# Kernel tuning notes

Measured on AMD Instinct MI355X. Metric: run time of the kernel, lower is better.

The kernel has to match this reference:

```python
import jax, jax.numpy as jnp
import numpy as np

N_NODES = 50000
N_EDGES = 800000
D_IN = 128
D_OUT = 128


def setup_inputs() -> dict:
    key = jax.random.key(0)
    ks = jax.random.split(key, 10)
    x = jax.random.normal(ks[0], (N_NODES, D_IN), dtype=jnp.float32)
    lp_rows = jax.random.randint(ks[1], (N_EDGES,), 0, N_NODES, dtype=jnp.int32)
    lp_cols = jax.random.randint(ks[2], (N_EDGES,), 0, N_NODES, dtype=jnp.int32)
    # low-pass operator: positive normalized-adjacency-like weights
    lp_vals = jax.random.uniform(ks[3], (N_EDGES,), dtype=jnp.float32) / 16.0
    hp_rows = jax.random.randint(ks[4], (N_EDGES,), 0, N_NODES, dtype=jnp.int32)
    hp_cols = jax.random.randint(ks[5], (N_EDGES,), 0, N_NODES, dtype=jnp.int32)
    # high-pass operator: signed (Laplacian-like) weights
    hp_vals = jax.random.normal(ks[6], (N_EDGES,), dtype=jnp.float32) / 16.0
    alpha_w = jax.random.normal(ks[7], (1, D_IN), dtype=jnp.float32) * 0.05
    alpha_b = jnp.zeros((1,), dtype=jnp.float32)
    W = jax.random.normal(ks[8], (D_OUT, D_IN), dtype=jnp.float32) * (1.0 / np.sqrt(D_IN))
    b = jnp.zeros((D_OUT,), dtype=jnp.float32)
    return {"x": x, "lp_rows": lp_rows, "lp_cols": lp_cols, "lp_vals": lp_vals,
            "hp_rows": hp_rows, "hp_cols": hp_cols, "hp_vals": hp_vals,
            "alpha_w": alpha_w, "alpha_b": alpha_b, "W": W, "b": b}


def _spmm(rows, cols, vals, x, n):
    # COO sparse-dense matmul: out[r] += vals[e] * x[cols[e]]
    return jax.ops.segment_sum(vals[:, None] * x[cols], rows, num_segments=n)


def reference(x, lp_rows, lp_cols, lp_vals, hp_rows, hp_cols, hp_vals,
              alpha_w, alpha_b, W, b):
    n = x.shape[0]
    # per-node mixing gate: alpha_i = sigmoid(x_i . theta + b)  -> [N, 1]
    alpha = jax.nn.sigmoid(x @ alpha_w.T + alpha_b)
    z_lp = _spmm(lp_rows, lp_cols, lp_vals, x, n)   # [N, D_IN]
    z_hp = _spmm(hp_rows, hp_cols, hp_vals, x, n)   # [N, D_IN]
    z_mix = alpha * z_lp + (1.0 - alpha) * z_hp
    out = jax.nn.relu(z_mix @ W.T + b)              # use_activation=True
    return out, alpha
```

## Files before the change

kernel.cpp:

```cpp
#include <hip/hip_runtime.h>

#define N_NODES_C 50000
#define N_EDGES_C 800000
#define N_EDGES2_C (2 * N_EDGES_C)
#define D 128
#define NSHARD 8
#define OFCAP 4096

#define BROWS 4
#define NBKT (N_NODES_C / BROWS)
#define NSB (NSHARD * NBKT)
#define BCAP 32

#define GNODES 64
#define LDP 132
#define GGRID ((N_NODES_C + GNODES - 1) / GNODES)
#define FGRID 2048
#define FEPB ((N_EDGES2_C + FGRID - 1) / FGRID)
#define TOTG (GGRID + FGRID)

static __device__ __forceinline__ unsigned short f2bf(float f) {
  unsigned u = __float_as_uint(f);
  u += 0x7fff + ((u >> 16) & 1);
  return (unsigned short)(u >> 16);
}
static __device__ __forceinline__ float bf_lo(unsigned u) {
  return __uint_as_float(u << 16);
}
static __device__ __forceinline__ float bf_hi(unsigned u) {
  return __uint_as_float(u & 0xffff0000u);
}

static __device__ __forceinline__ int xcd_id() {
  int v;
  asm volatile("s_getreg_b32 %0, hwreg(HW_REG_XCC_ID, 0, 4)" : "=s"(v));
  return v & (NSHARD - 1);
}

__global__ __launch_bounds__(256) void alpha_zero_kernel(
    const float* __restrict__ x,
    const float* __restrict__ aw,
    const float* __restrict__ ab,
    float* __restrict__ alpha_out,
    float* __restrict__ alpha_ws,
    int* __restrict__ bcursor,
    int n) {
  int gtid = blockIdx.x * blockDim.x + threadIdx.x;
  if (gtid < NSB + 64) bcursor[gtid] = 0;

  int wave = gtid >> 6;
  int lane = threadIdx.x & 63;
  if (wave >= n) return;
  const float* xr = x + (size_t)wave * D;
  float s = xr[lane] * aw[lane] + xr[lane + 64] * aw[lane + 64];
  #pragma unroll
  for (int off = 32; off > 0; off >>= 1)
    s += __shfl_down(s, off);
  if (lane == 0) {
    float a = 1.0f / (1.0f + __expf(-(s + ab[0])));
    alpha_out[wave] = a;
    alpha_ws[wave] = a;
  }
}

__global__ __launch_bounds__(256) void gemm_fill_kernel(
    const float* __restrict__ x,
    const float* __restrict__ W,
    unsigned* __restrict__ y,
    const int* __restrict__ lp_rows, const int* __restrict__ lp_cols,
    const float* __restrict__ lp_vals,
    const int* __restrict__ hp_rows, const int* __restrict__ hp_cols,
    const float* __restrict__ hp_vals,
    const float* __restrict__ alpha,
    int* __restrict__ bcursor,
    uint2* __restrict__ bins,
    int* __restrict__ ofcnt,
    uint2* __restrict__ ofl,
    int n) {
  __shared__ float zs[GNODES][LDP];
  __shared__ float wt[64][LDP];

  int t = threadIdx.x;
  int bid = blockIdx.x;
  int g = (bid * GGRID) / TOTG;
  int gn = ((bid + 1) * GGRID) / TOTG;

  if (gn > g) {
    int node0 = g * GNODES;
    int tn = t & 15;
    int tjg = t >> 4;
    int jb = tjg * 4;

    #pragma unroll
    for (int it = 0; it < 8; ++it) {
      int f = t + it * 256;
      int r = f >> 5;
      int c4 = f & 31;
      int node = node0 + r;
      float4 v = make_float4(0.f, 0.f, 0.f, 0.f);
      if (node < n) v = ((const float4*)(x + (size_t)node * D))[c4];
      *(float4*)&zs[r][c4 * 4] = v;
    }

    for (int jh = 0; jh < 2; ++jh) {
      if (jh) __syncthreads();
      #pragma unroll
      for (int it = 0; it < 8; ++it) {
        int f = t + it * 256;
        int j = f >> 5;
        int k4 = f & 31;
        *(float4*)&wt[j][k4 * 4] =
            ((const float4*)W)[(size_t)(jh * 64 + j) * 32 + k4];
      }
      __syncthreads();

      float acc[4][4] = {};
      #pragma unroll 2
      for (int k = 0; k < D; k += 4) {
        float4 w0 = *(const float4*)&wt[jb + 0][k];
        float4 w1 = *(const float4*)&wt[jb + 1][k];
        float4 w2 = *(const float4*)&wt[jb + 2][k];
        float4 w3 = *(const float4*)&wt[jb + 3][k];
        float4 z0 = *(const float4*)&zs[tn][k];
        float4 z1 = *(const float4*)&zs[tn + 16][k];
        float4 z2 = *(const float4*)&zs[tn + 32][k];
        float4 z3 = *(const float4*)&zs[tn + 48][k];
        acc[0][0] += z0.x*w0.x + z0.y*w0.y + z0.z*w0.z + z0.w*w0.w;
        acc[0][1] += z0.x*w1.x + z0.y*w1.y + z0.z*w1.z + z0.w*w1.w;
        acc[0][2] += z0.x*w2.x + z0.y*w2.y + z0.z*w2.z + z0.w*w2.w;
        acc[0][3] += z0.x*w3.x + z0.y*w3.y + z0.z*w3.z + z0.w*w3.w;
        acc[1][0] += z1.x*w0.x + z1.y*w0.y + z1.z*w0.z + z1.w*w0.w;
        acc[1][1] += z1.x*w1.x + z1.y*w1.y + z1.z*w1.z + z1.w*w1.w;
        acc[1][2] += z1.x*w2.x + z1.y*w2.y + z1.z*w2.z + z1.w*w2.w;
        acc[1][3] += z1.x*w3.x + z1.y*w3.y + z1.z*w3.z + z1.w*w3.w;
        acc[2][0] += z2.x*w0.x + z2.y*w0.y + z2.z*w0.z + z2.w*w0.w;
        acc[2][1] += z2.x*w1.x + z2.y*w1.y + z2.z*w1.z + z2.w*w1.w;
        acc[2][2] += z2.x*w2.x + z2.y*w2.y + z2.z*w2.z + z2.w*w2.w;
        acc[2][3] += z2.x*w3.x + z2.y*w3.y + z2.z*w3.z + z2.w*w3.w;
        acc[3][0] += z3.x*w0.x + z3.y*w0.y + z3.z*w0.z + z3.w*w0.w;
        acc[3][1] += z3.x*w1.x + z3.y*w1.y + z3.z*w1.z + z3.w*w1.w;
        acc[3][2] += z3.x*w2.x + z3.y*w2.y + z3.z*w2.z + z3.w*w2.w;
        acc[3][3] += z3.x*w3.x + z3.y*w3.y + z3.z*w3.z + z3.w*w3.w;
      }

      #pragma unroll
      for (int ii = 0; ii < 4; ++ii) {
        int node = node0 + ii * 16 + tn;
        if (node < n) {
          uint2 o;
          o.x = (unsigned)f2bf(acc[ii][0]) | ((unsigned)f2bf(acc[ii][1]) << 16);
          o.y = (unsigned)f2bf(acc[ii][2]) | ((unsigned)f2bf(acc[ii][3]) << 16);
          *(uint2*)&y[(size_t)node * 64 + jh * 32 + tjg * 2] = o;
        }
      }
    }
  } else {
    int fb = bid - g;
    int xcc = xcd_id();
    int e0 = fb * FEPB;
    int e1 = e0 + FEPB;
    if (e1 > N_EDGES2_C) e1 = N_EDGES2_C;
    for (int e = e0 + t; e < e1; e += 256) {
      int r, c;
      float v;
      if (e < N_EDGES_C) {
        r = __builtin_nontemporal_load(lp_rows + e);
        c = __builtin_nontemporal_load(lp_cols + e);
        v = __builtin_nontemporal_load(lp_vals + e) * alpha[r];
      } else {
        int i = e - N_EDGES_C;
        r = __builtin_nontemporal_load(hp_rows + i);
        c = __builtin_nontemporal_load(hp_cols + i);
        v = __builtin_nontemporal_load(hp_vals + i) * (1.0f - alpha[r]);
      }
      int sb = xcc * NBKT + (r >> 2);
      int p = atomicAdd(&bcursor[sb], 1);
      if (p < BCAP) {
        bins[(size_t)sb * BCAP + p] =
            make_uint2(((unsigned)r << 16) | (unsigned)c, __float_as_uint(v));
      } else {
        int q = atomicAdd(ofcnt, 1);
        if (q < OFCAP)
          ofl[q] = make_uint2(((unsigned)r << 16) | (unsigned)c,
                              (unsigned)__float_as_int(v));
      }
    }
  }
}

__global__ __launch_bounds__(256) void gather_kernel(
    const int* __restrict__ bcursor,
    const uint2* __restrict__ bins,
    const unsigned* __restrict__ y,
    const float* __restrict__ bias,
    const int* __restrict__ ofcnt,
    const uint2* __restrict__ ofl,
    float* __restrict__ out) {
  int t = threadIdx.x;
  int w = t >> 6;
  int lane = t & 63;
  int bkt = blockIdx.x * 4 + w;

  float a0L = 0.f, a0H = 0.f, a1L = 0.f, a1H = 0.f;
  float a2L = 0.f, a2H = 0.f, a3L = 0.f, a3H = 0.f;

  #define ACC(RR, VV, UU)                                        \
    do {                                                         \
      float uL_ = bf_lo(UU), uH_ = bf_hi(UU);                    \
      switch (RR) {                                              \
        case 0: a0L += (VV) * uL_; a0H += (VV) * uH_; break;     \
        case 1: a1L += (VV) * uL_; a1H += (VV) * uH_; break;     \
        case 2: a2L += (VV) * uL_; a2H += (VV) * uH_; break;     \
        default: a3L += (VV) * uL_; a3H += (VV) * uH_; break;    \
      }                                                          \
    } while (0)

  int cnts[8];
  uint2 wvs[8];
  #pragma unroll
  for (int s = 0; s < 8; ++s) {
    int c = bcursor[s * NBKT + bkt];
    cnts[s] = c > BCAP ? BCAP : c;
  }
  #pragma unroll
  for (int s = 0; s < 8; ++s) {
    wvs[s] = make_uint2(0u, 0u);
    if (lane < cnts[s])
      wvs[s] = bins[(size_t)(s * NBKT + bkt) * BCAP + lane];
  }

  #pragma unroll
  for (int s = 0; s < 8; ++s) {
    int cnt = cnts[s];
    uint2 wv = wvs[s];
    int i = 0;
    for (; i + 3 < cnt; i += 4) {
      unsigned x0 = (unsigned)__shfl((int)wv.x, i + 0);
      unsigned x1 = (unsigned)__shfl((int)wv.x, i + 1);
      unsigned x2 = (unsigned)__shfl((int)wv.x, i + 2);
      unsigned x3 = (unsigned)__shfl((int)wv.x, i + 3);
      float v0 = __uint_as_float((unsigned)__shfl((int)wv.y, i + 0));
      float v1 = __uint_as_float((unsigned)__shfl((int)wv.y, i + 1));
      float v2 = __uint_as_float((unsigned)__shfl((int)wv.y, i + 2));
      float v3 = __uint_as_float((unsigned)__shfl((int)wv.y, i + 3));
      unsigned u0 = y[(size_t)(x0 & 0xffffu) * 64 + lane];
      unsigned u1 = y[(size_t)(x1 & 0xffffu) * 64 + lane];
      unsigned u2 = y[(size_t)(x2 & 0xffffu) * 64 + lane];
      unsigned u3 = y[(size_t)(x3 & 0xffffu) * 64 + lane];
      int r0 = (int)__builtin_amdgcn_readfirstlane((x0 >> 16) & 3);
      int r1 = (int)__builtin_amdgcn_readfirstlane((x1 >> 16) & 3);
      int r2 = (int)__builtin_amdgcn_readfirstlane((x2 >> 16) & 3);
      int r3 = (int)__builtin_amdgcn_readfirstlane((x3 >> 16) & 3);
      ACC(r0, v0, u0);
      ACC(r1, v1, u1);
      ACC(r2, v2, u2);
      ACC(r3, v3, u3);
    }
    for (; i < cnt; ++i) {
      unsigned x0 = (unsigned)__shfl((int)wv.x, i);
      float v0 = __uint_as_float((unsigned)__shfl((int)wv.y, i));
      unsigned u0 = y[(size_t)(x0 & 0xffffu) * 64 + lane];
      int r0 = (int)__builtin_amdgcn_readfirstlane((x0 >> 16) & 3);
      ACC(r0, v0, u0);
    }
  }

  int nof = *ofcnt;
  if (nof > OFCAP) nof = OFCAP;
  for (int i = 0; i < nof; ++i) {
    uint2 o = ofl[i];
    unsigned r = o.x >> 16;
    if ((int)(r >> 2) == bkt) {
      unsigned u = y[(size_t)(o.x & 0xffffu) * 64 + lane];
      float v = __int_as_float((int)o.y);
      ACC((int)(r & 3), v, u);
    }
  }
  #undef ACC

  float2 bv = *(const float2*)&bias[lane * 2];
  size_t ro = (size_t)bkt * 4 * D + lane * 2;
  float2 o0, o1, o2, o3;
  o0.x = fmaxf(a0L + bv.x, 0.0f); o0.y = fmaxf(a0H + bv.y, 0.0f);
  o1.x = fmaxf(a1L + bv.x, 0.0f); o1.y = fmaxf(a1H + bv.y, 0.0f);
  o2.x = fmaxf(a2L + bv.x, 0.0f); o2.y = fmaxf(a2H + bv.y, 0.0f);
  o3.x = fmaxf(a3L + bv.x, 0.0f); o3.y = fmaxf(a3H + bv.y, 0.0f);
  *(float2*)&out[ro + 0 * D] = o0;
  *(float2*)&out[ro + 1 * D] = o1;
  *(float2*)&out[ro + 2 * D] = o2;
  *(float2*)&out[ro + 3 * D] = o3;
}

extern "C" void kernel_launch(void* const* d_in, const int* in_sizes, int n_in,
                              void* d_out, int out_size, void* d_ws, size_t ws_size,
                              hipStream_t stream) {
  const float* x = (const float*)d_in[0];
  const int* lp_rows = (const int*)d_in[1];
  const int* lp_cols = (const int*)d_in[2];
  const float* lp_vals = (const float*)d_in[3];
  const int* hp_rows = (const int*)d_in[4];
  const int* hp_cols = (const int*)d_in[5];
  const float* hp_vals = (const float*)d_in[6];
  const float* alpha_w = (const float*)d_in[7];
  const float* alpha_b = (const float*)d_in[8];
  const float* W = (const float*)d_in[9];
  const float* bias = (const float*)d_in[10];

  float* out = (float*)d_out;
  float* alpha_out = out + (size_t)N_NODES_C * D;

  char* ws = (char*)d_ws;
  unsigned* y = (unsigned*)ws;   ws += (size_t)N_NODES_C * 64 * 4;
  float* alpha_ws = (float*)ws;  ws += 200192;
  int* bcursor = (int*)ws;       ws += (size_t)NSB * 4;
  int* ofcnt = (int*)ws;         ws += 256;
  uint2* ofl = (uint2*)ws;       ws += (size_t)OFCAP * 8;
  uint2* bins = (uint2*)ws;
  ws += (size_t)NSB * BCAP * 8;

  alpha_zero_kernel<<<(N_NODES_C + 3) / 4, 256, 0, stream>>>(
      x, alpha_w, alpha_b, alpha_out, alpha_ws, bcursor, N_NODES_C);

  gemm_fill_kernel<<<TOTG, 256, 0, stream>>>(
      x, W, y,
      lp_rows, lp_cols, lp_vals, hp_rows, hp_cols, hp_vals,
      alpha_ws, bcursor, bins, ofcnt, ofl, N_NODES_C);

  gather_kernel<<<NBKT / 4, 256, 0, stream>>>(
      bcursor, bins, (const unsigned*)y, bias, ofcnt, ofl, out);
}
```

Baseline: 274.5 us.

## Fold alpha gate into GEMM blocks and apply alpha in gather via tag bit

Moves the per-node sigmoid gate computation out of the standalone first kernel and into the GEMM blocks of the fused gemm/fill kernel. The first kernel now only zeroes the bucket cursors with int4 stores. Edge values no longer carry alpha, which removes the random alpha[r] read during binning. Instead, the low bit of each stored value marks the edge as low-pass or high-pass, and the gather kernel multiplies by alpha or 1-alpha for the row it already owns. This lets the fill blocks run without waiting on the alpha computation, but it perturbs the value's lowest mantissa bit and adds a select and multiply per edge in the gather loop.

```diff
diff --git a/kernel.cpp b/kernel.cpp
--- a/kernel.cpp
+++ b/kernel.cpp
@@ -37,41 +37,23 @@
   return v & (NSHARD - 1);
 }
 
-__global__ __launch_bounds__(256) void alpha_zero_kernel(
+__global__ __launch_bounds__(256) void zero_kernel(int4* __restrict__ p) {
+  int g = blockIdx.x * 256 + threadIdx.x;
+  if (g < (NSB + 64) / 4) p[g] = make_int4(0, 0, 0, 0);
+}
+
+__global__ __launch_bounds__(256) void gemm_fill_kernel(
     const float* __restrict__ x,
+    const float* __restrict__ W,
     const float* __restrict__ aw,
     const float* __restrict__ ab,
     float* __restrict__ alpha_out,
     float* __restrict__ alpha_ws,
-    int* __restrict__ bcursor,
-    int n) {
-  int gtid = blockIdx.x * blockDim.x + threadIdx.x;
-  if (gtid < NSB + 64) bcursor[gtid] = 0;
-
-  int wave = gtid >> 6;
-  int lane = threadIdx.x & 63;
-  if (wave >= n) return;
-  const float* xr = x + (size_t)wave * D;
-  float s = xr[lane] * aw[lane] + xr[lane + 64] * aw[lane + 64];
-  #pragma unroll
-  for (int off = 32; off > 0; off >>= 1)
-    s += __shfl_down(s, off);
-  if (lane == 0) {
-    float a = 1.0f / (1.0f + __expf(-(s + ab[0])));
-    alpha_out[wave] = a;
-    alpha_ws[wave] = a;
-  }
-}
-
-__global__ __launch_bounds__(256) void gemm_fill_kernel(
-    const float* __restrict__ x,
-    const float* __restrict__ W,
     unsigned* __restrict__ y,
     const int* __restrict__ lp_rows, const int* __restrict__ lp_cols,
     const float* __restrict__ lp_vals,
     const int* __restrict__ hp_rows, const int* __restrict__ hp_cols,
     const float* __restrict__ hp_vals,
-    const float* __restrict__ alpha,
     int* __restrict__ bcursor,
     uint2* __restrict__ bins,
     int* __restrict__ ofcnt,
@@ -154,6 +136,25 @@
         }
       }
     }
+
+    int wv = t >> 6;
+    int ln = t & 63;
+    float bb = ab[0];
+    for (int ii = 0; ii < 16; ++ii) {
+      int node = node0 + wv * 16 + ii;
+      if (node < n) {
+        const float* xr = x + (size_t)node * D;
+        float s = xr[ln] * aw[ln] + xr[ln + 64] * aw[ln + 64];
+        #pragma unroll
+        for (int off = 32; off > 0; off >>= 1)
+          s += __shfl_down(s, off);
+        if (ln == 0) {
+          float a = 1.0f / (1.0f + __expf(-(s + bb)));
+          alpha_out[node] = a;
+          alpha_ws[node] = a;
+        }
+      }
+    }
   } else {
     int fb = bid - g;
     int xcc = xcd_id();
@@ -162,27 +163,26 @@
     if (e1 > N_EDGES2_C) e1 = N_EDGES2_C;
     for (int e = e0 + t; e < e1; e += 256) {
       int r, c;
-      float v;
+      unsigned vb;
       if (e < N_EDGES_C) {
         r = __builtin_nontemporal_load(lp_rows + e);
         c = __builtin_nontemporal_load(lp_cols + e);
-        v = __builtin_nontemporal_load(lp_vals + e) * alpha[r];
+        vb = (__float_as_uint(__builtin_nontemporal_load(lp_vals + e)) & ~1u) | 1u;
       } else {
         int i = e - N_EDGES_C;
         r = __builtin_nontemporal_load(hp_rows + i);
         c = __builtin_nontemporal_load(hp_cols + i);
-        v = __builtin_nontemporal_load(hp_vals + i) * (1.0f - alpha[r]);
+        vb = __float_as_uint(__builtin_nontemporal_load(hp_vals + i)) & ~1u;
       }
       int sb = xcc * NBKT + (r >> 2);
       int p = atomicAdd(&bcursor[sb], 1);
       if (p < BCAP) {
         bins[(size_t)sb * BCAP + p] =
-            make_uint2(((unsigned)r << 16) | (unsigned)c, __float_as_uint(v));
+            make_uint2(((unsigned)r << 16) | (unsigned)c, vb);
       } else {
         int q = atomicAdd(ofcnt, 1);
         if (q < OFCAP)
-          ofl[q] = make_uint2(((unsigned)r << 16) | (unsigned)c,
-                              (unsigned)__float_as_int(v));
+          ofl[q] = make_uint2(((unsigned)r << 16) | (unsigned)c, vb);
       }
     }
   }
@@ -193,6 +193,7 @@
     const uint2* __restrict__ bins,
     const unsigned* __restrict__ y,
     const float* __restrict__ bias,
+    const float* __restrict__ alpha_ws,
     const int* __restrict__ ofcnt,
     const uint2* __restrict__ ofl,
     float* __restrict__ out) {
@@ -201,18 +202,26 @@
   int lane = t & 63;
   int bkt = blockIdx.x * 4 + w;
 
+  const float* ap = alpha_ws + (size_t)bkt * 4;
+  float aA0 = ap[0], aA1 = ap[1], aA2 = ap[2], aA3 = ap[3];
+  float aB0 = 1.f - aA0, aB1 = 1.f - aA1, aB2 = 1.f - aA2, aB3 = 1.f - aA3;
+
   float a0L = 0.f, a0H = 0.f, a1L = 0.f, a1H = 0.f;
   float a2L = 0.f, a2H = 0.f, a3L = 0.f, a3H = 0.f;
 
-  #define ACC(RR, VV, UU)                                        \
-    do {                                                         \
-      float uL_ = bf_lo(UU), uH_ = bf_hi(UU);                    \
-      switch (RR) {                                              \
-        case 0: a0L += (VV) * uL_; a0H += (VV) * uH_; break;     \
-        case 1: a1L += (VV) * uL_; a1H += (VV) * uH_; break;     \
-        case 2: a2L += (VV) * uL_; a2H += (VV) * uH_; break;     \
-        default: a3L += (VV) * uL_; a3H += (VV) * uH_; break;    \
-      }                                                          \
+  #define ACC(RR, FF, VV, UU)                                               \
+    do {                                                                    \
+      float uL_ = bf_lo(UU), uH_ = bf_hi(UU);                               \
+      switch (RR) {                                                         \
+        case 0: { float vm_ = (VV) * ((FF) ? aA0 : aB0);                    \
+                  a0L += vm_ * uL_; a0H += vm_ * uH_; } break;              \
+        case 1: { float vm_ = (VV) * ((FF) ? aA1 : aB1);                    \
+                  a1L += vm_ * uL_; a1H += vm_ * uH_; } break;              \
+        case 2: { float vm_ = (VV) * ((FF) ? aA2 : aB2);                    \
+                  a2L += vm_ * uL_; a2H += vm_ * uH_; } break;              \
+        default:{ float vm_ = (VV) * ((FF) ? aA3 : aB3);                    \
+                  a3L += vm_ * uL_; a3H += vm_ * uH_; } break;              \
+      }                                                                     \
     } while (0)
 
   int cnts[8];
@@ -239,29 +248,34 @@
       unsigned x1 = (unsigned)__shfl((int)wv.x, i + 1);
       unsigned x2 = (unsigned)__shfl((int)wv.x, i + 2);
       unsigned x3 = (unsigned)__shfl((int)wv.x, i + 3);
-      float v0 = __uint_as_float((unsigned)__shfl((int)wv.y, i + 0));
-      float v1 = __uint_as_float((unsigned)__shfl((int)wv.y, i + 1));
-      float v2 = __uint_as_float((unsigned)__shfl((int)wv.y, i + 2));
-      float v3 = __uint_as_float((unsigned)__shfl((int)wv.y, i + 3));
+      unsigned vb0 = (unsigned)__shfl((int)wv.y, i + 0);
+      unsigned vb1 = (unsigned)__shfl((int)wv.y, i + 1);
+      unsigned vb2 = (unsigned)__shfl((int)wv.y, i + 2);
+      unsigned vb3 = (unsigned)__shfl((int)wv.y, i + 3);
       unsigned u0 = y[(size_t)(x0 & 0xffffu) * 64 + lane];
       unsigned u1 = y[(size_t)(x1 & 0xffffu) * 64 + lane];
       unsigned u2 = y[(size_t)(x2 & 0xffffu) * 64 + lane];
       unsigned u3 = y[(size_t)(x3 & 0xffffu) * 64 + lane];
+      float v0 = __uint_as_float(vb0 & ~1u);
+      float v1 = __uint_as_float(vb1 & ~1u);
+      float v2 = __uint_as_float(vb2 & ~1u);
+      float v3 = __uint_as_float(vb3 & ~1u);
       int r0 = (int)__builtin_amdgcn_readfirstlane((x0 >> 16) & 3);
       int r1 = (int)__builtin_amdgcn_readfirstlane((x1 >> 16) & 3);
       int r2 = (int)__builtin_amdgcn_readfirstlane((x2 >> 16) & 3);
       int r3 = (int)__builtin_amdgcn_readfirstlane((x3 >> 16) & 3);
-      ACC(r0, v0, u0);
-      ACC(r1, v1, u1);
-      ACC(r2, v2, u2);
-      ACC(r3, v3, u3);
+      ACC(r0, vb0 & 1u, v0, u0);
+      ACC(r1, vb1 & 1u, v1, u1);
+      ACC(r2, vb2 & 1u, v2, u2);
+      ACC(r3, vb3 & 1u, v3, u3);
     }
     for (; i < cnt; ++i) {
       unsigned x0 = (unsigned)__shfl((int)wv.x, i);
-      float v0 = __uint_as_float((unsigned)__shfl((int)wv.y, i));
+      unsigned vb0 = (unsigned)__shfl((int)wv.y, i);
       unsigned u0 = y[(size_t)(x0 & 0xffffu) * 64 + lane];
+      float v0 = __uint_as_float(vb0 & ~1u);
       int r0 = (int)__builtin_amdgcn_readfirstlane((x0 >> 16) & 3);
-      ACC(r0, v0, u0);
+      ACC(r0, vb0 & 1u, v0, u0);
     }
   }
 
@@ -272,8 +286,8 @@
     unsigned r = o.x >> 16;
     if ((int)(r >> 2) == bkt) {
       unsigned u = y[(size_t)(o.x & 0xffffu) * 64 + lane];
-      float v = __int_as_float((int)o.y);
-      ACC((int)(r & 3), v, u);
+      float v = __uint_as_float(o.y & ~1u);
+      ACC((int)(r & 3), o.y & 1u, v, u);
     }
   }
   #undef ACC
@@ -318,14 +332,14 @@
   uint2* bins = (uint2*)ws;
   ws += (size_t)NSB * BCAP * 8;
 
-  alpha_zero_kernel<<<(N_NODES_C + 3) / 4, 256, 0, stream>>>(
-      x, alpha_w, alpha_b, alpha_out, alpha_ws, bcursor, N_NODES_C);
+  zero_kernel<<<((NSB + 64) / 4 + 255) / 256, 256, 0, stream>>>(
+      (int4*)bcursor);
 
   gemm_fill_kernel<<<TOTG, 256, 0, stream>>>(
-      x, W, y,
+      x, W, alpha_w, alpha_b, alpha_out, alpha_ws, y,
       lp_rows, lp_cols, lp_vals, hp_rows, hp_cols, hp_vals,
-      alpha_ws, bcursor, bins, ofcnt, ofl, N_NODES_C);
+      bcursor, bins, ofcnt, ofl, N_NODES_C);
 
   gather_kernel<<<NBKT / 4, 256, 0, stream>>>(
-      bcursor, bins, (const unsigned*)y, bias, ofcnt, ofl, out);
-}
+      bcursor, bins, (const unsigned*)y, bias, alpha_ws, ofcnt, ofl, out);
+}
```

Result: slower. 287.8 us (+4.8%).

## Split gather bucket across eight waves, one per shard, with LDS reduction

Applied to the files above, without the earlier changes.

Gather now gives each 4-row bucket its own 512-thread block, with one wave per XCC shard. Before, a single wave walked all eight shards in sequence. Partial sums go into shared memory and are reduced by four waves, which apply bias and ReLU. This raises parallelism and memory-level concurrency for the latency-bound row gathers. In exchange it adds a block-wide barrier, LDS traffic and more blocks; with fewer waves per bucket the overflow scan now runs on wave 0 only.

```diff
diff --git a/kernel.cpp b/kernel.cpp
--- a/kernel.cpp
+++ b/kernel.cpp
@@ -188,7 +188,7 @@
   }
 }
 
-__global__ __launch_bounds__(256) void gather_kernel(
+__global__ __launch_bounds__(512) void gather_kernel(
     const int* __restrict__ bcursor,
     const uint2* __restrict__ bins,
     const unsigned* __restrict__ y,
@@ -196,10 +196,11 @@
     const int* __restrict__ ofcnt,
     const uint2* __restrict__ ofl,
     float* __restrict__ out) {
+  __shared__ float2 part[8][4][64];
   int t = threadIdx.x;
   int w = t >> 6;
   int lane = t & 63;
-  int bkt = blockIdx.x * 4 + w;
+  int bkt = blockIdx.x;
 
   float a0L = 0.f, a0H = 0.f, a1L = 0.f, a1H = 0.f;
   float a2L = 0.f, a2H = 0.f, a3L = 0.f, a3H = 0.f;
@@ -215,80 +216,78 @@
       }                                                          \
     } while (0)
 
-  int cnts[8];
-  uint2 wvs[8];
-  #pragma unroll
-  for (int s = 0; s < 8; ++s) {
-    int c = bcursor[s * NBKT + bkt];
-    cnts[s] = c > BCAP ? BCAP : c;
-  }
-  #pragma unroll
-  for (int s = 0; s < 8; ++s) {
-    wvs[s] = make_uint2(0u, 0u);
-    if (lane < cnts[s])
-      wvs[s] = bins[(size_t)(s * NBKT + bkt) * BCAP + lane];
-  }
-
-  #pragma unroll
-  for (int s = 0; s < 8; ++s) {
-    int cnt = cnts[s];
-    uint2 wv = wvs[s];
-    int i = 0;
-    for (; i + 3 < cnt; i += 4) {
-      unsigned x0 = (unsigned)__shfl((int)wv.x, i + 0);
-      unsigned x1 = (unsigned)__shfl((int)wv.x, i + 1);
-      unsigned x2 = (unsigned)__shfl((int)wv.x, i + 2);
-      unsigned x3 = (unsigned)__shfl((int)wv.x, i + 3);
-      float v0 = __uint_as_float((unsigned)__shfl((int)wv.y, i + 0));
-      float v1 = __uint_as_float((unsigned)__shfl((int)wv.y, i + 1));
-      float v2 = __uint_as_float((unsigned)__shfl((int)wv.y, i + 2));
-      float v3 = __uint_as_float((unsigned)__shfl((int)wv.y, i + 3));
-      unsigned u0 = y[(size_t)(x0 & 0xffffu) * 64 + lane];
-      unsigned u1 = y[(size_t)(x1 & 0xffffu) * 64 + lane];
-      unsigned u2 = y[(size_t)(x2 & 0xffffu) * 64 + lane];
-      unsigned u3 = y[(size_t)(x3 & 0xffffu) * 64 + lane];
-      int r0 = (int)__builtin_amdgcn_readfirstlane((x0 >> 16) & 3);
-      int r1 = (int)__builtin_amdgcn_readfirstlane((x1 >> 16) & 3);
-      int r2 = (int)__builtin_amdgcn_readfirstlane((x2 >> 16) & 3);
-      int r3 = (int)__builtin_amdgcn_readfirstlane((x3 >> 16) & 3);
-      ACC(r0, v0, u0);
-      ACC(r1, v1, u1);
-      ACC(r2, v2, u2);
-      ACC(r3, v3, u3);
-    }
-    for (; i < cnt; ++i) {
-      unsigned x0 = (unsigned)__shfl((int)wv.x, i);
-      float v0 = __uint_as_float((unsigned)__shfl((int)wv.y, i));
-      unsigned u0 = y[(size_t)(x0 & 0xffffu) * 64 + lane];
-      int r0 = (int)__builtin_amdgcn_readfirstlane((x0 >> 16) & 3);
-      ACC(r0, v0, u0);
-    }
-  }
-
-  int nof = *ofcnt;
-  if (nof > OFCAP) nof = OFCAP;
-  for (int i = 0; i < nof; ++i) {
-    uint2 o = ofl[i];
-    unsigned r = o.x >> 16;
-    if ((int)(r >> 2) == bkt) {
-      unsigned u = y[(size_t)(o.x & 0xffffu) * 64 + lane];
-      float v = __int_as_float((int)o.y);
-      ACC((int)(r & 3), v, u);
+  int sb = w * NBKT + bkt;
+  int cnt = bcursor[sb];
+  if (cnt > BCAP) cnt = BCAP;
+  uint2 wv = make_uint2(0u, 0u);
+  if (lane < cnt) wv = bins[(size_t)sb * BCAP + lane];
+
+  int i = 0;
+  for (; i + 3 < cnt; i += 4) {
+    unsigned x0 = (unsigned)__shfl((int)wv.x, i + 0);
+    unsigned x1 = (unsigned)__shfl((int)wv.x, i + 1);
+    unsigned x2 = (unsigned)__shfl((int)wv.x, i + 2);
+    unsigned x3 = (unsigned)__shfl((int)wv.x, i + 3);
+    float v0 = __uint_as_float((unsigned)__shfl((int)wv.y, i + 0));
+    float v1 = __uint_as_float((unsigned)__shfl((int)wv.y, i + 1));
+    float v2 = __uint_as_float((unsigned)__shfl((int)wv.y, i + 2));
+    float v3 = __uint_as_float((unsigned)__shfl((int)wv.y, i + 3));
+    unsigned u0 = y[(size_t)(x0 & 0xffffu) * 64 + lane];
+    unsigned u1 = y[(size_t)(x1 & 0xffffu) * 64 + lane];
+    unsigned u2 = y[(size_t)(x2 & 0xffffu) * 64 + lane];
+    unsigned u3 = y[(size_t)(x3 & 0xffffu) * 64 + lane];
+    int r0 = (int)__builtin_amdgcn_readfirstlane((x0 >> 16) & 3);
+    int r1 = (int)__builtin_amdgcn_readfirstlane((x1 >> 16) & 3);
+    int r2 = (int)__builtin_amdgcn_readfirstlane((x2 >> 16) & 3);
+    int r3 = (int)__builtin_amdgcn_readfirstlane((x3 >> 16) & 3);
+    ACC(r0, v0, u0);
+    ACC(r1, v1, u1);
+    ACC(r2, v2, u2);
+    ACC(r3, v3, u3);
+  }
+  for (; i < cnt; ++i) {
+    unsigned x0 = (unsigned)__shfl((int)wv.x, i);
+    float v0 = __uint_as_float((unsigned)__shfl((int)wv.y, i));
+    unsigned u0 = y[(size_t)(x0 & 0xffffu) * 64 + lane];
+    int r0 = (int)__builtin_amdgcn_readfirstlane((x0 >> 16) & 3);
+    ACC(r0, v0, u0);
+  }
+
+  if (w == 0) {
+    int nof = *ofcnt;
+    if (nof > OFCAP) nof = OFCAP;
+    for (int k = 0; k < nof; ++k) {
+      uint2 o = ofl[k];
+      unsigned r = o.x >> 16;
+      if ((int)(r >> 2) == bkt) {
+        unsigned u = y[(size_t)(o.x & 0xffffu) * 64 + lane];
+        float v = __uint_as_float(o.y);
+        ACC((int)(r & 3), v, u);
+      }
     }
   }
   #undef ACC
 
-  float2 bv = *(const float2*)&bias[lane * 2];
-  size_t ro = (size_t)bkt * 4 * D + lane * 2;
-  float2 o0, o1, o2, o3;
-  o0.x = fmaxf(a0L + bv.x, 0.0f); o0.y = fmaxf(a0H + bv.y, 0.0f);
-  o1.x = fmaxf(a1L + bv.x, 0.0f); o1.y = fmaxf(a1H + bv.y, 0.0f);
-  o2.x = fmaxf(a2L + bv.x, 0.0f); o2.y = fmaxf(a2H + bv.y, 0.0f);
-  o3.x = fmaxf(a3L + bv.x, 0.0f); o3.y = fmaxf(a3H + bv.y, 0.0f);
-  *(float2*)&out[ro + 0 * D] = o0;
-  *(float2*)&out[ro + 1 * D] = o1;
-  *(float2*)&out[ro + 2 * D] = o2;
-  *(float2*)&out[ro + 3 * D] = o3;
+  part[w][0][lane] = make_float2(a0L, a0H);
+  part[w][1][lane] = make_float2(a1L, a1H);
+  part[w][2][lane] = make_float2(a2L, a2H);
+  part[w][3][lane] = make_float2(a3L, a3H);
+  __syncthreads();
+
+  if (w < 4) {
+    float sL = 0.f, sH = 0.f;
+    #pragma unroll
+    for (int s = 0; s < 8; ++s) {
+      float2 p = part[s][w][lane];
+      sL += p.x;
+      sH += p.y;
+    }
+    float2 bv = *(const float2*)&bias[lane * 2];
+    float2 o;
+    o.x = fmaxf(sL + bv.x, 0.0f);
+    o.y = fmaxf(sH + bv.y, 0.0f);
+    *(float2*)&out[(size_t)(bkt * 4 + w) * D + lane * 2] = o;
+  }
 }
 
 extern "C" void kernel_launch(void* const* d_in, const int* in_sizes, int n_in,
@@ -326,6 +325,6 @@
       lp_rows, lp_cols, lp_vals, hp_rows, hp_cols, hp_vals,
       alpha_ws, bcursor, bins, ofcnt, ofl, N_NODES_C);
 
-  gather_kernel<<<NBKT / 4, 256, 0, stream>>>(
+  gather_kernel<<<NBKT, 512, 0, stream>>>(
       bcursor, bins, (const unsigned*)y, bias, ofcnt, ofl, out);
 }
```

Result: slower. 289.8 us (+5.6%).
